# Optimization experiments

Hardware: AMD Instinct MI355X
Metric: run time of the kernel (lower is better)

## Reference

```python
import jax, jax.numpy as jnp
import numpy as np

N_NODES = 100000
N_EDGES = 1600000
IN_DIM = 128
HID = 128
FC_DIM = 64
OUT_DIM = 1
NUM_LAYERS = 8
NUM_GRAPHS = 128
EPS = 1e-5


def _layernorm(x, gamma, beta):
    mu = jnp.mean(x, axis=-1, keepdims=True)
    var = jnp.mean(jnp.square(x - mu), axis=-1, keepdims=True)
    return (x - mu) * jax.lax.rsqrt(var + EPS) * gamma + beta


def _gcn_conv(x, row, col, W, b):
    # PyG GCNConv: h = X W; out[v] = sum_{(u,v)} norm(u,v) h[u] + b
    # self-loops already appended to row/col, norms precomputable per call
    n = x.shape[0]
    deg = jnp.zeros((n,), x.dtype).at[col].add(jnp.ones((row.shape[0],), x.dtype))
    dinv = jnp.where(deg > 0, jax.lax.rsqrt(deg), 0.0)
    norm = dinv[row] * dinv[col]                      # [E+N]
    h = x @ W                                         # [N, H]
    out = jnp.zeros((n, W.shape[1]), x.dtype).at[col].add(norm[:, None] * h[row])
    return out + b


def _block(x, row, col, W, b, g, be):
    return jax.nn.relu(_layernorm(_gcn_conv(x, row, col, W, b), g, be))


def setup_inputs() -> dict:
    key = jax.random.key(0)
    ks = jax.random.split(key, 16)
    x = jax.random.normal(ks[0], (N_NODES, IN_DIM), jnp.float32)
    edge_index = jax.random.randint(ks[1], (2, N_EDGES), 0, N_NODES, jnp.int32)
    batch = jnp.sort(jax.random.randint(ks[2], (N_NODES,), 0, NUM_GRAPHS, jnp.int32))

    def lin(k, fan_in, fan_out):
        s = 1.0 / np.sqrt(fan_in)
        return jax.random.uniform(k, (fan_in, fan_out), jnp.float32, -s, s)

    return {
        "x": x, "edge_index": edge_index, "batch": batch,
        "W_in": lin(ks[3], IN_DIM, HID), "b_in": jnp.zeros((HID,), jnp.float32),
        "g_in": jnp.ones((HID,), jnp.float32), "be_in": jnp.zeros((HID,), jnp.float32),
        "W_mid": lin(ks[4], HID, HID), "b_mid": jnp.zeros((HID,), jnp.float32),
        "g_mid": jnp.ones((HID,), jnp.float32), "be_mid": jnp.zeros((HID,), jnp.float32),
        "W_out": lin(ks[5], HID, HID), "b_out": jnp.zeros((HID,), jnp.float32),
        "g_out": jnp.ones((HID,), jnp.float32), "be_out": jnp.zeros((HID,), jnp.float32),
        "W1": lin(ks[6], HID, FC_DIM), "b1": jnp.zeros((FC_DIM,), jnp.float32),
        "W2": lin(ks[7], FC_DIM, OUT_DIM), "b2": jnp.zeros((OUT_DIM,), jnp.float32),
    }


def reference(x, edge_index, batch,
              W_in, b_in, g_in, be_in,
              W_mid, b_mid, g_mid, be_mid,
              W_out, b_out, g_out, be_out,
              W1, b1, W2, b2):
    n = x.shape[0]
    sl = jnp.arange(n, dtype=edge_index.dtype)
    row = jnp.concatenate([edge_index[0], sl])   # sources (+ self loops)
    col = jnp.concatenate([edge_index[1], sl])   # targets (+ self loops)

    # layer 0
    h = _block(x, row, col, W_in, b_in, g_in, be_in)
    # layers 1..num_layers-2 share middle_conv params; even idx adds residual
    for i in range(1, NUM_LAYERS - 1):
        if i % 2 == 0:
            h = _block(h, row, col, W_mid, b_mid, g_mid, be_mid) + h
        else:
            h = _block(h, row, col, W_mid, b_mid, g_mid, be_mid)
    # last layer
    h = _block(h, row, col, W_out, b_out, g_out, be_out)

    # global mean pool over batch ids
    ones = jnp.ones((n, 1), h.dtype)
    sums = jnp.zeros((NUM_GRAPHS, HID), h.dtype).at[batch].add(h)
    cnts = jnp.zeros((NUM_GRAPHS, 1), h.dtype).at[batch].add(ones)
    pooled = sums / jnp.maximum(cnts, 1.0)

    z = jax.nn.relu(pooled @ W1 + b1)            # dropout = identity (eval)
    return jax.nn.sigmoid(z @ W2 + b2)
```

## Files before the change

kernel.cpp:

```cpp
#include <hip/hip_runtime.h>
#include <hip/hip_fp16.h>

#define NN 100000
#define NE 1600000
#define DIM 128
#define NGRAPH 128
#define FCD 64

#define NBK 391
#define ECH 8192
#define NCH 196
#define ECAP 8192

typedef _Float16 half_t;
typedef _Float16 half2_t __attribute__((ext_vector_type(2)));
typedef _Float16 half4_t __attribute__((ext_vector_type(4)));

__device__ inline half2_t u2h(unsigned u) { union { unsigned u; half2_t h; } x; x.u = u; return x.h; }
__device__ inline unsigned h2u(half2_t h) { union { unsigned u; half2_t h; } x; x.h = h; return x.u; }

#if defined(__has_builtin)
#if __has_builtin(__builtin_amdgcn_fdot2)
#define HAS_FDOT2 1
#endif
#endif
#ifndef HAS_FDOT2
#define HAS_FDOT2 0
#endif

__device__ inline float dot2(half2_t a, half2_t b, float c) {
#if HAS_FDOT2
  return __builtin_amdgcn_fdot2(a, b, c, false);
#else
  return c + (float)a[0] * (float)b[0] + (float)a[1] * (float)b[1];
#endif
}

__global__ __launch_bounds__(256) void k_bucketA(const int* __restrict__ row,
                                                 const int* __restrict__ col,
                                                 int* __restrict__ staged,
                                                 int* __restrict__ offmat,
                                                 int* __restrict__ gtot) {
  __shared__ int hist[NBK];
  __shared__ int sc[512];
  __shared__ int off[NBK + 1];
  __shared__ int fill[NBK];
  int b = blockIdx.x, t = threadIdx.x;
  int e0 = b * ECH;
  int n = NE - e0; if (n > ECH) n = ECH;
  for (int j = t; j < NBK; j += 256) { hist[j] = 0; fill[j] = 0; }
  __syncthreads();
  for (int i = t; i < n; i += 256) atomicAdd(&hist[col[e0 + i] >> 8], 1);
  __syncthreads();
  sc[t] = (t < NBK) ? hist[t] : 0;
  sc[t + 256] = (t + 256 < NBK) ? hist[t + 256] : 0;
  __syncthreads();
  #pragma unroll
  for (int o = 1; o < 512; o <<= 1) {
    int a0 = (t >= o) ? sc[t - o] : 0;
    int a1 = (t + 256 >= o) ? sc[t + 256 - o] : 0;
    __syncthreads();
    sc[t] += a0; sc[t + 256] += a1;
    __syncthreads();
  }
  if (t == 0) off[0] = 0;
  for (int j = t; j < NBK; j += 256) off[j + 1] = sc[j];
  for (int j = t; j < NBK; j += 256) if (hist[j]) atomicAdd(&gtot[j], hist[j]);
  __syncthreads();
  for (int j = t; j < NBK + 1; j += 256) offmat[b * (NBK + 1) + j] = off[j];
  for (int i = t; i < n; i += 256) {
    int c = col[e0 + i], r = row[e0 + i];
    int bkt = c >> 8;
    int pos = off[bkt] + atomicAdd(&fill[bkt], 1);
    staged[e0 + pos] = (r << 8) | (c & 255);
  }
}

__global__ void k_bsum(const int* __restrict__ gtot, int* __restrict__ gbase,
                       int* __restrict__ rowptr) {
  __shared__ int sc[512];
  int t = threadIdx.x;
  sc[t] = (t < NBK) ? gtot[t] : 0;
  sc[t + 256] = (t + 256 < NBK) ? gtot[t + 256] : 0;
  __syncthreads();
  #pragma unroll
  for (int o = 1; o < 512; o <<= 1) {
    int a0 = (t >= o) ? sc[t - o] : 0;
    int a1 = (t + 256 >= o) ? sc[t + 256 - o] : 0;
    __syncthreads();
    sc[t] += a0; sc[t + 256] += a1;
    __syncthreads();
  }
  if (t == 0) { gbase[0] = 0; rowptr[NN] = NE; }
  for (int j = t; j < NBK; j += 256) gbase[j + 1] = sc[j];
}

__global__ __launch_bounds__(256) void k_csrB(const int* __restrict__ staged,
                                              const int* __restrict__ offmat,
                                              const int* __restrict__ gbase,
                                              int* __restrict__ rowptr,
                                              float* __restrict__ dinv,
                                              int* __restrict__ csrc) {
  __shared__ int pay[ECAP];
  __shared__ int csn[256];
  __shared__ int nhist[256];
  __shared__ int nscan[256];
  __shared__ int nb[256];
  __shared__ int nfill[256];
  int bkt = blockIdx.x, t = threadIdx.x;
  int gb = gbase[bkt];
  int off = 0, cnt = 0;
  if (t < NCH) {
    int base = t * (NBK + 1) + bkt;
    off = offmat[base];
    cnt = offmat[base + 1] - off;
  }
  csn[t] = cnt;
  __syncthreads();
  #pragma unroll
  for (int o = 1; o < 256; o <<= 1) {
    int a = (t >= o) ? csn[t - o] : 0;
    __syncthreads();
    csn[t] += a;
    __syncthreads();
  }
  int lb = csn[t] - cnt;
  int total = csn[255];
  if (t < NCH) {
    const int* src = staged + t * ECH + off;
    for (int i = 0; i < cnt; i++) pay[lb + i] = src[i];
  }
  nhist[t] = 0; nfill[t] = 0;
  __syncthreads();
  for (int i = t; i < total; i += 256) atomicAdd(&nhist[pay[i] & 255], 1);
  __syncthreads();
  nscan[t] = nhist[t];
  __syncthreads();
  #pragma unroll
  for (int o = 1; o < 256; o <<= 1) {
    int a = (t >= o) ? nscan[t - o] : 0;
    __syncthreads();
    nscan[t] += a;
    __syncthreads();
  }
  nb[t] = nscan[t] - nhist[t];
  int v = bkt * 256 + t;
  if (v < NN) {
    rowptr[v] = gb + nb[t];
    dinv[v] = rsqrtf((float)(nhist[t] + 1));
  }
  __syncthreads();
  for (int i = t; i < total; i += 256) {
    int p = pay[i];
    int cl = p & 255;
    int pos = nb[cl] + atomicAdd(&nfill[cl], 1);
    csrc[gb + pos] = p >> 8;
  }
}

__global__ void k_cvt(const float* __restrict__ x, half_t* __restrict__ Xh) {
  int i = blockIdx.x * 256 + threadIdx.x;
  if ((size_t)i * 4 < (size_t)NN * DIM) {
    float4 v = *(const float4*)&x[(size_t)i * 4];
    half4_t h; h[0] = (half_t)v.x; h[1] = (half_t)v.y; h[2] = (half_t)v.z; h[3] = (half_t)v.w;
    *(half4_t*)&Xh[(size_t)i * 4] = h;
  }
}

__global__ __launch_bounds__(256) void k_gemm(const half_t* __restrict__ X,
                                              const float* __restrict__ W,
                                              const float* __restrict__ dinv,
                                              half_t* __restrict__ O) {
  __shared__ unsigned Xs[32 * 68];
  __shared__ unsigned Ws[32 * 144];
  int n0 = blockIdx.x * 64;
  int t = threadIdx.x;
  int tx = t & 15, ty = t >> 4;
  float acc[4][8] = {};
  for (int kb = 0; kb < 128; kb += 64) {
    __syncthreads();
    #pragma unroll
    for (int i = 0; i < 2; i++) {
      int e = t + i * 256;
      int row = e >> 3;
      int seg = e & 7;
      int n = n0 + row;
      uint4 v = make_uint4(0, 0, 0, 0);
      if (n < NN) v = *(const uint4*)&X[(size_t)n * DIM + kb + seg * 8];
      int kp0 = seg * 4;
      Xs[(kp0 + 0) * 68 + row] = v.x;
      Xs[(kp0 + 1) * 68 + row] = v.y;
      Xs[(kp0 + 2) * 68 + row] = v.z;
      Xs[(kp0 + 3) * 68 + row] = v.w;
    }
    #pragma unroll
    for (int i = 0; i < 4; i++) {
      int e = t + i * 256;
      int kp = e >> 5;
      int j0 = (e & 31) * 4;
      float4 a = *(const float4*)&W[(size_t)(kb + 2 * kp) * DIM + j0];
      float4 b = *(const float4*)&W[(size_t)(kb + 2 * kp + 1) * DIM + j0];
      half2_t p0; p0[0] = (half_t)a.x; p0[1] = (half_t)b.x;
      half2_t p1; p1[0] = (half_t)a.y; p1[1] = (half_t)b.y;
      half2_t p2; p2[0] = (half_t)a.z; p2[1] = (half_t)b.z;
      half2_t p3; p3[0] = (half_t)a.w; p3[1] = (half_t)b.w;
      int off = j0 + (j0 >> 3);
      *(uint4*)&Ws[kp * 144 + off] = make_uint4(h2u(p0), h2u(p1), h2u(p2), h2u(p3));
    }
    __syncthreads();
    #pragma unroll 4
    for (int kp = 0; kp < 32; kp++) {
      uint4 au = *(const uint4*)&Xs[kp * 68 + ty * 4];
      uint4 b0 = *(const uint4*)&Ws[kp * 144 + tx * 9];
      uint4 b1 = *(const uint4*)&Ws[kp * 144 + tx * 9 + 4];
      half2_t a[4] = { u2h(au.x), u2h(au.y), u2h(au.z), u2h(au.w) };
      half2_t b[8] = { u2h(b0.x), u2h(b0.y), u2h(b0.z), u2h(b0.w),
                       u2h(b1.x), u2h(b1.y), u2h(b1.z), u2h(b1.w) };
      #pragma unroll
      for (int r = 0; r < 4; r++)
        #pragma unroll
        for (int c = 0; c < 8; c++)
          acc[r][c] = dot2(a[r], b[c], acc[r][c]);
    }
  }
  #pragma unroll
  for (int r = 0; r < 4; r++) {
    int n = n0 + ty * 4 + r;
    if (n < NN) {
      float dv = dinv[n];
      half2_t h[4];
      #pragma unroll
      for (int c = 0; c < 4; c++) {
        half2_t p; p[0] = (half_t)(acc[r][2 * c] * dv); p[1] = (half_t)(acc[r][2 * c + 1] * dv);
        h[c] = p;
      }
      uint4 o4 = make_uint4(h2u(h[0]), h2u(h[1]), h2u(h[2]), h2u(h[3]));
      *(uint4*)&O[(size_t)n * DIM + tx * 8] = o4;
    }
  }
}

__global__ __launch_bounds__(256) void k_agg(const half2_t* __restrict__ Hh,
                      half2_t* __restrict__ Ah,
                      const int* __restrict__ rowptr, const int* __restrict__ csrc,
                      const float* __restrict__ dinv,
                      const float* __restrict__ bias, const float* __restrict__ gamma,
                      const float* __restrict__ beta, int res) {
  int tid = threadIdx.x;
  int lane = tid & 63;
  int v = blockIdx.x * 4 + (tid >> 6);
  int g = lane >> 4;
  int fl = lane & 15;
  int s0 = rowptr[v];
  int cnt = rowptr[v + 1] - s0;
  const uint4* Hq = (const uint4*)Hh;
  half2_t a0 = u2h(0u), a1 = u2h(0u), a2 = u2h(0u), a3 = u2h(0u);
  for (int i = g; i < cnt; i += 16) {
    int j1 = i + 4, j2 = i + 8, j3 = i + 12;
    int c1 = min(j1, cnt - 1);
    int c2 = min(j2, cnt - 1);
    int c3 = min(j3, cnt - 1);
    int e0 = csrc[s0 + i];
    int e1 = csrc[s0 + c1];
    int e2 = csrc[s0 + c2];
    int e3 = csrc[s0 + c3];
    uint4 q0 = Hq[(size_t)e0 * 16 + fl];
    uint4 q1 = Hq[(size_t)e1 * 16 + fl];
    uint4 q2 = Hq[(size_t)e2 * 16 + fl];
    uint4 q3 = Hq[(size_t)e3 * 16 + fl];
    a0 += u2h(q0.x); a1 += u2h(q0.y); a2 += u2h(q0.z); a3 += u2h(q0.w);
    if (j1 < cnt) { a0 += u2h(q1.x); a1 += u2h(q1.y); a2 += u2h(q1.z); a3 += u2h(q1.w); }
    if (j2 < cnt) { a0 += u2h(q2.x); a1 += u2h(q2.y); a2 += u2h(q2.z); a3 += u2h(q2.w); }
    if (j3 < cnt) { a0 += u2h(q3.x); a1 += u2h(q3.y); a2 += u2h(q3.z); a3 += u2h(q3.w); }
  }
  float f0 = (float)a0[0], f1 = (float)a0[1], f2 = (float)a1[0], f3 = (float)a1[1];
  float f4 = (float)a2[0], f5 = (float)a2[1], f6 = (float)a3[0], f7 = (float)a3[1];
  f0 += __shfl_xor(f0, 16); f0 += __shfl_xor(f0, 32);
  f1 += __shfl_xor(f1, 16); f1 += __shfl_xor(f1, 32);
  f2 += __shfl_xor(f2, 16); f2 += __shfl_xor(f2, 32);
  f3 += __shfl_xor(f3, 16); f3 += __shfl_xor(f3, 32);
  f4 += __shfl_xor(f4, 16); f4 += __shfl_xor(f4, 32);
  f5 += __shfl_xor(f5, 16); f5 += __shfl_xor(f5, 32);
  f6 += __shfl_xor(f6, 16); f6 += __shfl_xor(f6, 32);
  f7 += __shfl_xor(f7, 16); f7 += __shfl_xor(f7, 32);
  uint4 qs = Hq[(size_t)v * 16 + fl];
  half2_t s0h = u2h(qs.x), s1h = u2h(qs.y), s2h = u2h(qs.z), s3h = u2h(qs.w);
  f0 += (float)s0h[0]; f1 += (float)s0h[1]; f2 += (float)s1h[0]; f3 += (float)s1h[1];
  f4 += (float)s2h[0]; f5 += (float)s2h[1]; f6 += (float)s3h[0]; f7 += (float)s3h[1];
  float dv = dinv[v];
  float4 ba = *(const float4*)&bias[fl * 8];
  float4 bb = *(const float4*)&bias[fl * 8 + 4];
  f0 = f0 * dv + ba.x; f1 = f1 * dv + ba.y; f2 = f2 * dv + ba.z; f3 = f3 * dv + ba.w;
  f4 = f4 * dv + bb.x; f5 = f5 * dv + bb.y; f6 = f6 * dv + bb.z; f7 = f7 * dv + bb.w;
  float s  = ((f0 + f1) + (f2 + f3)) + ((f4 + f5) + (f6 + f7));
  float ss = ((f0 * f0 + f1 * f1) + (f2 * f2 + f3 * f3))
           + ((f4 * f4 + f5 * f5) + (f6 * f6 + f7 * f7));
  #pragma unroll
  for (int o = 1; o < 16; o <<= 1) { s += __shfl_xor(s, o); ss += __shfl_xor(ss, o); }
  float mu = s * (1.f / 128.f);
  float var = ss * (1.f / 128.f) - mu * mu;
  float rs = rsqrtf(var + 1e-5f);
  float pa = (g == 0) ? f0 : (g == 1) ? f2 : (g == 2) ? f4 : f6;
  float pb = (g == 0) ? f1 : (g == 1) ? f3 : (g == 2) ? f5 : f7;
  int fi = fl * 8 + g * 2;
  float2 g2 = *(const float2*)&gamma[fi];
  float2 e2 = *(const float2*)&beta[fi];
  float y0 = fmaxf((pa - mu) * rs * g2.x + e2.x, 0.f);
  float y1 = fmaxf((pb - mu) * rs * g2.y + e2.y, 0.f);
  half2_t* Ap = &Ah[(size_t)v * 64 + (fi >> 1)];
  if (res) { half2_t o2 = *Ap; y0 += (float)o2[0]; y1 += (float)o2[1]; }
  half2_t w; w[0] = (half_t)y0; w[1] = (half_t)y1;
  *Ap = w;
}

__global__ __launch_bounds__(64) void k_pool(const half2_t* __restrict__ Ah,
                                             const int* __restrict__ batch,
                                             float* __restrict__ sums) {
  const int CH = 64;
  int b0 = blockIdx.x * CH;
  int t = threadIdx.x;
  int nmax = NN - b0; if (nmax > CH) nmax = CH;
  __shared__ int bb[CH];
  bb[t] = (b0 + t < NN) ? batch[b0 + t] : -1;
  __syncthreads();
  int gfirst = bb[0], glast = bb[nmax - 1];
  if (gfirst == glast) {
    float p0 = 0.f, p1 = 0.f, q0 = 0.f, q1 = 0.f, r0 = 0.f, r1 = 0.f, u0 = 0.f, u1 = 0.f;
    int i = 0;
    for (; i + 4 <= nmax; i += 4) {
      half2_t h0 = Ah[(size_t)(b0 + i + 0) * 64 + t];
      half2_t h1 = Ah[(size_t)(b0 + i + 1) * 64 + t];
      half2_t h2 = Ah[(size_t)(b0 + i + 2) * 64 + t];
      half2_t h3 = Ah[(size_t)(b0 + i + 3) * 64 + t];
      p0 += (float)h0[0]; p1 += (float)h0[1];
      q0 += (float)h1[0]; q1 += (float)h1[1];
      r0 += (float)h2[0]; r1 += (float)h2[1];
      u0 += (float)h3[0]; u1 += (float)h3[1];
    }
    for (; i < nmax; ++i) {
      half2_t h = Ah[(size_t)(b0 + i) * 64 + t];
      p0 += (float)h[0]; p1 += (float)h[1];
    }
    atomicAdd(&sums[gfirst * DIM + 2 * t], (p0 + q0) + (r0 + u0));
    atomicAdd(&sums[gfirst * DIM + 2 * t + 1], (p1 + q1) + (r1 + u1));
  } else {
    float s0 = 0.f, s1 = 0.f;
    int cur = gfirst;
    for (int i = 0; i < nmax; i++) {
      int g = bb[i];
      if (g != cur) {
        atomicAdd(&sums[cur * DIM + 2 * t], s0);
        atomicAdd(&sums[cur * DIM + 2 * t + 1], s1);
        s0 = s1 = 0.f; cur = g;
      }
      half2_t h = Ah[(size_t)(b0 + i) * 64 + t];
      s0 += (float)h[0]; s1 += (float)h[1];
    }
    atomicAdd(&sums[cur * DIM + 2 * t], s0);
    atomicAdd(&sums[cur * DIM + 2 * t + 1], s1);
  }
}

__global__ void k_cnts(const int* __restrict__ batch, float* __restrict__ cnts) {
  int g = threadIdx.x;
  int lo = 0, hi = NN;
  while (lo < hi) { int mid = (lo + hi) >> 1; if (batch[mid] < g) lo = mid + 1; else hi = mid; }
  int a = lo;
  lo = 0; hi = NN;
  while (lo < hi) { int mid = (lo + hi) >> 1; if (batch[mid] < g + 1) lo = mid + 1; else hi = mid; }
  cnts[g] = (float)(lo - a);
}

__global__ void k_head(const float* __restrict__ sums, const float* __restrict__ cnts,
                       const float* __restrict__ W1, const float* __restrict__ b1,
                       const float* __restrict__ W2, const float* __restrict__ b2,
                       float* __restrict__ out) {
  int g = blockIdx.x, t = threadIdx.x;
  __shared__ float p[128];
  float ic = 1.f / fmaxf(cnts[g], 1.f);
  p[t] = sums[g * DIM + t] * ic;
  p[t + 64] = sums[g * DIM + 64 + t] * ic;
  __syncthreads();
  float z = b1[t];
  #pragma unroll 8
  for (int k = 0; k < 128; k++) z += p[k] * W1[k * FCD + t];
  z = fmaxf(z, 0.f);
  float sv = z * W2[t];
  #pragma unroll
  for (int o = 1; o < 64; o <<= 1) sv += __shfl_xor(sv, o);
  if (t == 0) out[g] = 1.f / (1.f + expf(-(sv + b2[0])));
}

extern "C" void kernel_launch(void* const* d_in, const int* in_sizes, int n_in,
                              void* d_out, int out_size, void* d_ws, size_t ws_size,
                              hipStream_t stream) {
  (void)in_sizes; (void)n_in; (void)out_size; (void)ws_size;
  const float* x     = (const float*)d_in[0];
  const int*   ei    = (const int*)d_in[1];
  const int*   batch = (const int*)d_in[2];
  const float* W_in  = (const float*)d_in[3];
  const float* b_in  = (const float*)d_in[4];
  const float* g_in  = (const float*)d_in[5];
  const float* be_in = (const float*)d_in[6];
  const float* W_mid = (const float*)d_in[7];
  const float* b_mid = (const float*)d_in[8];
  const float* g_mid = (const float*)d_in[9];
  const float* be_mid= (const float*)d_in[10];
  const float* W_out = (const float*)d_in[11];
  const float* b_out = (const float*)d_in[12];
  const float* g_out = (const float*)d_in[13];
  const float* be_out= (const float*)d_in[14];
  const float* W1    = (const float*)d_in[15];
  const float* b1    = (const float*)d_in[16];
  const float* W2    = (const float*)d_in[17];
  const float* b2    = (const float*)d_in[18];
  float* out = (float*)d_out;

  char* p = (char*)d_ws;
  auto alloc = [&](size_t bytes) {
    char* r = p;
    p += (bytes + 255) & ~(size_t)255;
    return r;
  };
  half_t* Ah     = (half_t*)alloc((size_t)NN * DIM * 2);
  half_t* Xh     = (half_t*)alloc((size_t)NN * DIM * 2);
  half_t* Bh     = (half_t*)alloc((size_t)NN * DIM * 2);
  float*  dinv   = (float*)alloc((size_t)NN * 4);
  int*    rowptr = (int*)alloc((size_t)(NN + 1) * 4);
  int*    csrc   = (int*)alloc((size_t)NE * 4);
  int*    staged = (int*)alloc((size_t)NCH * ECH * 4);
  int*    offmat = (int*)alloc((size_t)NCH * (NBK + 1) * 4);
  int*    gtot   = (int*)alloc((size_t)(NBK + 1) * 4);
  int*    gbase  = (int*)alloc((size_t)(NBK + 1) * 4);
  float*  sums   = (float*)alloc((size_t)NGRAPH * DIM * 4);
  float*  cnts   = (float*)alloc((size_t)NGRAPH * 4);

  const int* rowp = ei;
  const int* colp = ei + NE;

  hipMemsetAsync(gtot, 0, (size_t)(NBK + 1) * 4, stream);
  hipMemsetAsync(sums, 0, (size_t)NGRAPH * DIM * 4, stream);

  k_bucketA<<<NCH, 256, 0, stream>>>(rowp, colp, staged, offmat, gtot);
  k_bsum<<<1, 256, 0, stream>>>(gtot, gbase, rowptr);
  k_csrB<<<NBK, 256, 0, stream>>>(staged, offmat, gbase, rowptr, dinv, csrc);
  k_cvt<<<(NN * DIM / 4 + 255) / 256, 256, 0, stream>>>(x, Xh);

  int gemm_grid = (NN + 63) / 64;
  for (int l = 0; l < 8; l++) {
    const float *Wl, *bl, *gl, *bel;
    if (l == 0)      { Wl = W_in;  bl = b_in;  gl = g_in;  bel = be_in;  }
    else if (l == 7) { Wl = W_out; bl = b_out; gl = g_out; bel = be_out; }
    else             { Wl = W_mid; bl = b_mid; gl = g_mid; bel = be_mid; }
    const half_t* in = (l == 0) ? Xh : Ah;
    k_gemm<<<gemm_grid, 256, 0, stream>>>(in, Wl, dinv, Bh);
    int res = (l >= 2 && l <= 6 && (l % 2 == 0)) ? 1 : 0;
    k_agg<<<NN / 4, 256, 0, stream>>>((const half2_t*)Bh, (half2_t*)Ah,
                                      rowptr, csrc, dinv, bl, gl, bel, res);
  }

  k_pool<<<(NN + 63) / 64, 64, 0, stream>>>((const half2_t*)Ah, batch, sums);
  k_cnts<<<1, 128, 0, stream>>>(batch, cnts);
  k_head<<<NGRAPH, 64, 0, stream>>>(sums, cnts, W1, b1, W2, b2, out);
}
```

Before: 930.9 us.

## Use MFMA 16x16x32 f16 for per-layer GEMM with pre-transposed half weights

Replaces the dot2-based LDS-tiled GEMM with a wavefront-level MFMA kernel. X fragments are loaded straight from global memory into registers, and the weight matrices are converted and transposed to fp16 once up front. Output is staged through LDS so that global writes are coalesced 16-byte stores, and each block now covers 128 rows. This targets the GEMM's FP16 compute cost at the price of an extra transpose pre-pass and about 50KB of LDS per block.

```diff
diff --git a/kernel.cpp b/kernel.cpp
--- a/kernel.cpp
+++ b/kernel.cpp
@@ -15,26 +15,12 @@
 typedef _Float16 half_t;
 typedef _Float16 half2_t __attribute__((ext_vector_type(2)));
 typedef _Float16 half4_t __attribute__((ext_vector_type(4)));
+typedef _Float16 half8_t __attribute__((ext_vector_type(8)));
+typedef float float4_t __attribute__((ext_vector_type(4)));
 
 __device__ inline half2_t u2h(unsigned u) { union { unsigned u; half2_t h; } x; x.u = u; return x.h; }
 __device__ inline unsigned h2u(half2_t h) { union { unsigned u; half2_t h; } x; x.h = h; return x.u; }
-
-#if defined(__has_builtin)
-#if __has_builtin(__builtin_amdgcn_fdot2)
-#define HAS_FDOT2 1
-#endif
-#endif
-#ifndef HAS_FDOT2
-#define HAS_FDOT2 0
-#endif
-
-__device__ inline float dot2(half2_t a, half2_t b, float c) {
-#if HAS_FDOT2
-  return __builtin_amdgcn_fdot2(a, b, c, false);
-#else
-  return c + (float)a[0] * (float)b[0] + (float)a[1] * (float)b[1];
-#endif
-}
+__device__ inline half8_t q2h8(uint4 q) { union { uint4 q; half8_t h; } x; x.q = q; return x.h; }
 
 __global__ __launch_bounds__(256) void k_bucketA(const int* __restrict__ row,
                                                  const int* __restrict__ col,
@@ -167,75 +153,74 @@
   }
 }
 
+__global__ void k_wt(const float* __restrict__ W, half_t* __restrict__ Wt) {
+  int e = blockIdx.x * 256 + threadIdx.x;
+  if (e < DIM * DIM) {
+    int j = e >> 7, k = e & 127;
+    Wt[e] = (half_t)W[k * DIM + j];
+  }
+}
+
+#define WT_DW 66
 __global__ __launch_bounds__(256) void k_gemm(const half_t* __restrict__ X,
-                                              const float* __restrict__ W,
+                                              const uint4* __restrict__ Wtg,
                                               const float* __restrict__ dinv,
                                               half_t* __restrict__ O) {
-  __shared__ unsigned Xs[32 * 68];
-  __shared__ unsigned Ws[32 * 144];
-  int n0 = blockIdx.x * 64;
+  __shared__ unsigned wt[DIM * WT_DW];
+  __shared__ half_t outs[4][16 * 136];
   int t = threadIdx.x;
-  int tx = t & 15, ty = t >> 4;
-  float acc[4][8] = {};
-  for (int kb = 0; kb < 128; kb += 64) {
-    __syncthreads();
+  int w = t >> 6, l = t & 63;
+  #pragma unroll
+  for (int i = 0; i < 8; i++) {
+    int e = t + i * 256;
+    int j = e >> 4, seg = e & 15;
+    *(uint4*)&wt[j * WT_DW + seg * 4] = Wtg[e];
+  }
+  __syncthreads();
+  int lr = l & 15, lk = l >> 4;
+  #pragma unroll
+  for (int t4 = 0; t4 < 2; t4++) {
+    int n0w = blockIdx.x * 128 + w * 32 + t4 * 16;
+    int nA = n0w + lr;
+    uint4 a0 = make_uint4(0,0,0,0), a1 = a0, a2 = a0, a3 = a0;
+    if (nA < NN) {
+      const uint4* Xq = (const uint4*)&X[(size_t)nA * DIM];
+      a0 = Xq[lk];  a1 = Xq[4 + lk];  a2 = Xq[8 + lk];  a3 = Xq[12 + lk];
+    }
+    float4_t acc[8] = {};
     #pragma unroll
-    for (int i = 0; i < 2; i++) {
-      int e = t + i * 256;
-      int row = e >> 3;
-      int seg = e & 7;
-      int n = n0 + row;
-      uint4 v = make_uint4(0, 0, 0, 0);
-      if (n < NN) v = *(const uint4*)&X[(size_t)n * DIM + kb + seg * 8];
-      int kp0 = seg * 4;
-      Xs[(kp0 + 0) * 68 + row] = v.x;
-      Xs[(kp0 + 1) * 68 + row] = v.y;
-      Xs[(kp0 + 2) * 68 + row] = v.z;
-      Xs[(kp0 + 3) * 68 + row] = v.w;
-    }
+    for (int jt = 0; jt < 8; jt++) {
+      int bbase = (jt * 16 + lr) * WT_DW + lk * 4;
+      uint4 b0 = *(const uint4*)&wt[bbase];
+      uint4 b1 = *(const uint4*)&wt[bbase + 16];
+      uint4 b2 = *(const uint4*)&wt[bbase + 32];
+      uint4 b3 = *(const uint4*)&wt[bbase + 48];
+      acc[jt] = __builtin_amdgcn_mfma_f32_16x16x32_f16(q2h8(a0), q2h8(b0), acc[jt], 0, 0, 0);
+      acc[jt] = __builtin_amdgcn_mfma_f32_16x16x32_f16(q2h8(a1), q2h8(b1), acc[jt], 0, 0, 0);
+      acc[jt] = __builtin_amdgcn_mfma_f32_16x16x32_f16(q2h8(a2), q2h8(b2), acc[jt], 0, 0, 0);
+      acc[jt] = __builtin_amdgcn_mfma_f32_16x16x32_f16(q2h8(a3), q2h8(b3), acc[jt], 0, 0, 0);
+    }
+    float dv0 = dinv[min(n0w + lk * 4 + 0, NN - 1)];
+    float dv1 = dinv[min(n0w + lk * 4 + 1, NN - 1)];
+    float dv2 = dinv[min(n0w + lk * 4 + 2, NN - 1)];
+    float dv3 = dinv[min(n0w + lk * 4 + 3, NN - 1)];
     #pragma unroll
-    for (int i = 0; i < 4; i++) {
-      int e = t + i * 256;
-      int kp = e >> 5;
-      int j0 = (e & 31) * 4;
-      float4 a = *(const float4*)&W[(size_t)(kb + 2 * kp) * DIM + j0];
-      float4 b = *(const float4*)&W[(size_t)(kb + 2 * kp + 1) * DIM + j0];
-      half2_t p0; p0[0] = (half_t)a.x; p0[1] = (half_t)b.x;
-      half2_t p1; p1[0] = (half_t)a.y; p1[1] = (half_t)b.y;
-      half2_t p2; p2[0] = (half_t)a.z; p2[1] = (half_t)b.z;
-      half2_t p3; p3[0] = (half_t)a.w; p3[1] = (half_t)b.w;
-      int off = j0 + (j0 >> 3);
-      *(uint4*)&Ws[kp * 144 + off] = make_uint4(h2u(p0), h2u(p1), h2u(p2), h2u(p3));
-    }
-    __syncthreads();
-    #pragma unroll 4
-    for (int kp = 0; kp < 32; kp++) {
-      uint4 au = *(const uint4*)&Xs[kp * 68 + ty * 4];
-      uint4 b0 = *(const uint4*)&Ws[kp * 144 + tx * 9];
-      uint4 b1 = *(const uint4*)&Ws[kp * 144 + tx * 9 + 4];
-      half2_t a[4] = { u2h(au.x), u2h(au.y), u2h(au.z), u2h(au.w) };
-      half2_t b[8] = { u2h(b0.x), u2h(b0.y), u2h(b0.z), u2h(b0.w),
-                       u2h(b1.x), u2h(b1.y), u2h(b1.z), u2h(b1.w) };
-      #pragma unroll
-      for (int r = 0; r < 4; r++)
-        #pragma unroll
-        for (int c = 0; c < 8; c++)
-          acc[r][c] = dot2(a[r], b[c], acc[r][c]);
-    }
-  }
-  #pragma unroll
-  for (int r = 0; r < 4; r++) {
-    int n = n0 + ty * 4 + r;
-    if (n < NN) {
-      float dv = dinv[n];
-      half2_t h[4];
-      #pragma unroll
-      for (int c = 0; c < 4; c++) {
-        half2_t p; p[0] = (half_t)(acc[r][2 * c] * dv); p[1] = (half_t)(acc[r][2 * c + 1] * dv);
-        h[c] = p;
+    for (int jt = 0; jt < 8; jt++) {
+      int cb = jt * 16 + lr;
+      outs[w][(lk * 4 + 0) * 136 + cb] = (half_t)(acc[jt][0] * dv0);
+      outs[w][(lk * 4 + 1) * 136 + cb] = (half_t)(acc[jt][1] * dv1);
+      outs[w][(lk * 4 + 2) * 136 + cb] = (half_t)(acc[jt][2] * dv2);
+      outs[w][(lk * 4 + 3) * 136 + cb] = (half_t)(acc[jt][3] * dv3);
+    }
+    #pragma unroll
+    for (int q = 0; q < 4; q++) {
+      int idx = l * 4 + q;
+      int row = idx >> 4, seg = idx & 15;
+      int n = n0w + row;
+      if (n < NN) {
+        uint4 o4 = *(const uint4*)&outs[w][row * 136 + seg * 8];
+        *(uint4*)&O[(size_t)n * DIM + seg * 8] = o4;
       }
-      uint4 o4 = make_uint4(h2u(h[0]), h2u(h[1]), h2u(h[2]), h2u(h[3]));
-      *(uint4*)&O[(size_t)n * DIM + tx * 8] = o4;
     }
   }
 }
@@ -425,6 +410,7 @@
   half_t* Ah     = (half_t*)alloc((size_t)NN * DIM * 2);
   half_t* Xh     = (half_t*)alloc((size_t)NN * DIM * 2);
   half_t* Bh     = (half_t*)alloc((size_t)NN * DIM * 2);
+  half_t* Wt3    = (half_t*)alloc((size_t)3 * DIM * DIM * 2);
   float*  dinv   = (float*)alloc((size_t)NN * 4);
   int*    rowptr = (int*)alloc((size_t)(NN + 1) * 4);
   int*    csrc   = (int*)alloc((size_t)NE * 4);
@@ -445,15 +431,19 @@
   k_bsum<<<1, 256, 0, stream>>>(gtot, gbase, rowptr);
   k_csrB<<<NBK, 256, 0, stream>>>(staged, offmat, gbase, rowptr, dinv, csrc);
   k_cvt<<<(NN * DIM / 4 + 255) / 256, 256, 0, stream>>>(x, Xh);
-
-  int gemm_grid = (NN + 63) / 64;
+  k_wt<<<(DIM * DIM + 255) / 256, 256, 0, stream>>>(W_in,  Wt3);
+  k_wt<<<(DIM * DIM + 255) / 256, 256, 0, stream>>>(W_mid, Wt3 + DIM * DIM);
+  k_wt<<<(DIM * DIM + 255) / 256, 256, 0, stream>>>(W_out, Wt3 + 2 * DIM * DIM);
+
+  int gemm_grid = (NN + 127) / 128;
   for (int l = 0; l < 8; l++) {
-    const float *Wl, *bl, *gl, *bel;
-    if (l == 0)      { Wl = W_in;  bl = b_in;  gl = g_in;  bel = be_in;  }
-    else if (l == 7) { Wl = W_out; bl = b_out; gl = g_out; bel = be_out; }
-    else             { Wl = W_mid; bl = b_mid; gl = g_mid; bel = be_mid; }
+    const half_t* Wtl;
+    const float *bl, *gl, *bel;
+    if (l == 0)      { Wtl = Wt3;                 bl = b_in;  gl = g_in;  bel = be_in;  }
+    else if (l == 7) { Wtl = Wt3 + 2 * DIM * DIM; bl = b_out; gl = g_out; bel = be_out; }
+    else             { Wtl = Wt3 + DIM * DIM;     bl = b_mid; gl = g_mid; bel = be_mid; }
     const half_t* in = (l == 0) ? Xh : Ah;
-    k_gemm<<<gemm_grid, 256, 0, stream>>>(in, Wl, dinv, Bh);
+    k_gemm<<<gemm_grid, 256, 0, stream>>>(in, (const uint4*)Wtl, dinv, Bh);
     int res = (l >= 2 && l <= 6 && (l % 2 == 0)) ? 1 : 0;
     k_agg<<<NN / 4, 256, 0, stream>>>((const half2_t*)Bh, (half2_t*)Ah,
                                       rowptr, csrc, dinv, bl, gl, bel, res);
```

Result: faster. 760.5 us (-18.3%).
